# Optimization experiments

Hardware: AMD Instinct MI355X
Metric: run time of the kernel (lower is better)

Reference implementation:

```python
import jax, jax.numpy as jnp
import numpy as np

N_QUBITS = 8
N_LAYERS = 4
BATCH = 8192


def _ry_mat(theta):
    # RY(theta) = [[cos(t/2), -sin(t/2)], [sin(t/2), cos(t/2)]]; theta scalar or (B,)
    c = jnp.cos(theta * 0.5)
    s = jnp.sin(theta * 0.5)
    return jnp.stack([jnp.stack([c, -s], -1), jnp.stack([s, c], -1)], -2).astype(jnp.complex64)


def _apply_1q(state, U, wire):
    # U: (2,2) gate shared across batch; state: (B, 2,...,2) with axis wire+1 = target wire
    s = jnp.moveaxis(state, wire + 1, -1)
    s = jnp.einsum('ij,...j->...i', U, s)
    return jnp.moveaxis(s, -1, wire + 1)


def _apply_1q_batched(state, U, wire):
    # U: (B,2,2) per-sample gate (data-dependent RY angles)
    s = jnp.moveaxis(state, wire + 1, -1)
    s = jnp.einsum('bij,b...j->b...i', U, s)
    return jnp.moveaxis(s, -1, wire + 1)


def _apply_rz(state, theta, wire):
    # RZ is diagonal: multiply amplitudes by exp(-i t/2) / exp(+i t/2)
    phases = jnp.stack([jnp.exp(-0.5j * theta), jnp.exp(0.5j * theta)]).astype(jnp.complex64)
    s = jnp.moveaxis(state, wire + 1, -1)
    s = s * phases
    return jnp.moveaxis(s, -1, wire + 1)


def _cnot(state, c, t):
    # flip target amplitudes on the control=1 subspace
    s = jnp.moveaxis(state, (c + 1, t + 1), (-2, -1))
    s = jnp.stack([s[..., 0, :], s[..., 1, ::-1]], axis=-2)
    return jnp.moveaxis(s, (-2, -1), (c + 1, t + 1))


def _forward(x, weights):
    B = x.shape[0]
    state = jnp.zeros((B,) + (2,) * N_QUBITS, jnp.complex64)
    state = state.at[(slice(None),) + (0,) * N_QUBITS].set(1.0)  # |0...0>
    # data-encoding RY layer (angles depend on inputs -> per-sample gates)
    for i in range(N_QUBITS):
        state = _apply_1q_batched(state, _ry_mat(x[:, i] + weights[0, i, 0]), i)
    # entangling + rotation layers
    for layer in range(N_LAYERS):
        for i in range(N_QUBITS - 1):
            state = _cnot(state, i, i + 1)
        state = _cnot(state, N_QUBITS - 1, 0)
        for i in range(N_QUBITS):
            state = _apply_rz(state, weights[layer, i, 1], i)
            state = _apply_1q(state, _ry_mat(weights[layer, i, 0]), i)
    # <Z_i> = p(wire_i = 0) - p(wire_i = 1)
    p = state.real ** 2 + state.imag ** 2
    all_axes = tuple(range(1, N_QUBITS + 1))
    outs = []
    for i in range(N_QUBITS):
        m = p.sum(axis=tuple(a for a in all_axes if a != i + 1))  # (B, 2)
        outs.append(m[:, 0] - m[:, 1])
    return jnp.stack(outs, axis=1)  # (B, N_QUBITS)


def setup_inputs() -> dict:
    key = jax.random.key(0)
    k1, k2 = jax.random.split(key)
    x = jax.random.normal(k1, (BATCH, N_QUBITS), jnp.float32)
    weights = jax.random.normal(k2, (N_LAYERS, N_QUBITS, 2), jnp.float32)
    return {"x": x, "weights": weights}


def reference(x, weights):
    return _forward(x, weights)
```

## Files before the change

kernel.cpp:

```cpp
#include <hip/hip_runtime.h>

#define BATCH 8192

typedef __attribute__((ext_vector_type(8))) short bf16x8;
typedef __attribute__((ext_vector_type(4))) float f32x4;

__device__ __forceinline__ unsigned short f2bf(float f) {
    unsigned int u = __float_as_uint(f);
    u += 0x7fffu + ((u >> 16) & 1u);
    return (unsigned short)(u >> 16);
}
__device__ __forceinline__ float rfl(float v) {
    return __int_as_float(__builtin_amdgcn_readfirstlane(__float_as_int(v)));
}

__global__ __launch_bounds__(256) void ukern(const float* __restrict__ w,
                                             unsigned short* __restrict__ Ub)
{
    const int l = threadIdx.x & 63;
    const int c = blockIdx.x * 4 + (threadIdx.x >> 6);
    float re[4], im[4];
    const bool ls = (l == (c >> 2));
    #pragma unroll
    for (int k = 0; k < 4; ++k) {
        re[k] = (ls && ((c & 3) == k)) ? 1.0f : 0.0f;
        im[k] = 0.0f;
    }
    const int  src = (l ^ (l >> 1)) & 63;
    const bool c5  = (l & 1);
    #pragma unroll 1
    for (int layer = 0; layer < 4; ++layer) {
        const float* wl = w + layer * 16;
        float tr[4], ti[4];
        #pragma unroll
        for (int k = 0; k < 4; ++k) {
            tr[k] = __shfl(re[k], src, 64);
            ti[k] = __shfl(im[k], src, 64);
        }
        re[0] = c5 ? tr[2] : tr[0];  im[0] = c5 ? ti[2] : ti[0];
        re[1] = c5 ? tr[3] : tr[1];  im[1] = c5 ? ti[3] : ti[1];
        re[2] = c5 ? tr[1] : tr[3];  im[2] = c5 ? ti[1] : ti[3];
        re[3] = c5 ? tr[0] : tr[2];  im[3] = c5 ? ti[0] : ti[2];
        re[1] = __shfl_xor(re[1], 32, 64); im[1] = __shfl_xor(im[1], 32, 64);
        re[3] = __shfl_xor(re[3], 32, 64); im[3] = __shfl_xor(im[3], 32, 64);
        #pragma unroll
        for (int i = 0; i < 6; ++i) {
            float cth = __cosf(0.5f * wl[2*i]),   sth = __sinf(0.5f * wl[2*i]);
            float cph = __cosf(0.5f * wl[2*i+1]), sph = __sinf(0.5f * wl[2*i+1]);
            float Ar = rfl(cth * cph), SZ = rfl(sth * sph);
            float sgn = (l & (32 >> i)) ? 1.0f : -1.0f;
            float Ai = sgn * rfl(cth * sph);
            float Br = sgn * rfl(sth * cph);
            const int m = 32 >> i;
            #pragma unroll
            for (int k = 0; k < 4; ++k) {
                float br = __shfl_xor(re[k], m, 64);
                float bi = __shfl_xor(im[k], m, 64);
                float ar = re[k], ai = im[k];
                re[k] = Ar*ar - Ai*ai + Br*br + SZ*bi;
                im[k] = Ar*ai + Ai*ar + Br*bi - SZ*br;
            }
        }
        #pragma unroll
        for (int i = 0; i < 2; ++i) {
            float cy = rfl(__cosf(0.5f * wl[12 + 2*i]));
            float sy = rfl(__sinf(0.5f * wl[12 + 2*i]));
            float cf = rfl(__cosf(wl[13 + 2*i]));
            float sf = rfl(__sinf(wl[13 + 2*i]));
            const int mk = 2 >> i;
            #pragma unroll
            for (int k = 0; k < 4; ++k) {
                if (!(k & mk)) continue;
                float r = re[k], q = im[k];
                re[k] = r * cf - q * sf;
                im[k] = q * cf + r * sf;
            }
            #pragma unroll
            for (int k = 0; k < 4; ++k) {
                if (k & mk) continue;
                int k1 = k | mk;
                float ar = re[k], ai = im[k], br = re[k1], bi = im[k1];
                re[k]  = cy * ar - sy * br;
                im[k]  = cy * ai - sy * bi;
                re[k1] = sy * ar + cy * br;
                im[k1] = sy * ai + cy * bi;
            }
        }
    }
    #pragma unroll
    for (int k = 0; k < 4; ++k) {
        int i = l * 4 + k;
        Ub[i * 256 + c]         = f2bf(re[k]);
        Ub[(256 + i) * 256 + c] = f2bf(im[k]);
    }
}

__global__ __launch_bounds__(512) void qmain(const float* __restrict__ x,
                                             const float* __restrict__ w,
                                             const unsigned short* __restrict__ Ub,
                                             float* __restrict__ out)
{
    __shared__ float trg[32][17];
    __shared__ unsigned short psi[32 * 264];
    __shared__ float Ps[32][289];
    const int tid  = threadIdx.x;
    const int wid  = tid >> 6;
    const int lane = tid & 63;
    const int bid  = blockIdx.x;
    const int s0   = bid * 32;

    if (tid < 256) {
        const int s  = tid >> 3;
        const int wi = tid & 7;
        float a = 0.5f * (x[(s0 + s) * 8 + wi] + w[2 * wi]);
        trg[s][wi]     = __cosf(a);
        trg[s][8 + wi] = __sinf(a);
    }
    __syncthreads();

    {
        const int s  = tid >> 4;
        const int j1 = tid & 15;
        float c0 = trg[s][0], c1 = trg[s][1], c2 = trg[s][2], c3 = trg[s][3];
        float s0w = trg[s][8], s1w = trg[s][9], s2w = trg[s][10], s3w = trg[s][11];
        float A1 = ((j1 & 8) ? s0w : c0) * ((j1 & 4) ? s1w : c1)
                 * ((j1 & 2) ? s2w : c2) * ((j1 & 1) ? s3w : c3);
        float c4 = trg[s][4], c5 = trg[s][5], c6 = trg[s][6], c7 = trg[s][7];
        float s4 = trg[s][12], s5 = trg[s][13], s6 = trg[s][14], s7 = trg[s][15];
        float q45[4] = {A1 * c4 * c5, A1 * c4 * s5, A1 * s4 * c5, A1 * s4 * s5};
        float p67[4] = {c6 * c7, c6 * s7, s6 * c7, s6 * s7};
        unsigned int wbuf[8];
        #pragma unroll
        for (int p = 0; p < 8; ++p) {
            int ja = 2 * p, jb = 2 * p + 1;
            float va = q45[ja >> 2] * p67[ja & 3];
            float vb = q45[jb >> 2] * p67[jb & 3];
            wbuf[p] = (unsigned int)f2bf(va) | ((unsigned int)f2bf(vb) << 16);
        }
        uint4* dst = (uint4*)((char*)psi + s * 528 + j1 * 32);
        dst[0] = make_uint4(wbuf[0], wbuf[1], wbuf[2], wbuf[3]);
        dst[1] = make_uint4(wbuf[4], wbuf[5], wbuf[6], wbuf[7]);
    }
    __syncthreads();

    const int mrow = lane & 15;
    const int kgrp = lane >> 4;

    f32x4 acc[4][2];
    #pragma unroll
    for (int a = 0; a < 4; ++a)
        #pragma unroll
        for (int b = 0; b < 2; ++b)
            acc[a][b] = (f32x4){0.f, 0.f, 0.f, 0.f};

    #pragma unroll
    for (int ks = 0; ks < 8; ++ks) {
        const int k0 = ks * 32 + kgrp * 8;
        bf16x8 bfr0 = *(const bf16x8*)(psi + mrow * 264 + k0);
        bf16x8 bfr1 = *(const bf16x8*)(psi + (16 + mrow) * 264 + k0);
        #pragma unroll
        for (int mt = 0; mt < 4; ++mt) {
            const int row = (mt < 2) ? (wid * 32 + mt * 16 + mrow)
                                     : (256 + wid * 32 + (mt - 2) * 16 + mrow);
            bf16x8 afr = *(const bf16x8*)(Ub + row * 256 + k0);
            acc[mt][0] = __builtin_amdgcn_mfma_f32_16x16x32_bf16(afr, bfr0, acc[mt][0], 0, 0, 0);
            acc[mt][1] = __builtin_amdgcn_mfma_f32_16x16x32_bf16(afr, bfr1, acc[mt][1], 0, 0, 0);
        }
    }

    const int ct = wid * 4 + kgrp;
    #pragma unroll
    for (int nt = 0; nt < 2; ++nt) {
        float am[2], r2m[2], r1m[2];
        #pragma unroll
        for (int mtl = 0; mtl < 2; ++mtl) {
            float p0 = acc[mtl][nt][0]*acc[mtl][nt][0] + acc[mtl+2][nt][0]*acc[mtl+2][nt][0];
            float p1 = acc[mtl][nt][1]*acc[mtl][nt][1] + acc[mtl+2][nt][1]*acc[mtl+2][nt][1];
            float p2 = acc[mtl][nt][2]*acc[mtl][nt][2] + acc[mtl+2][nt][2]*acc[mtl+2][nt][2];
            float p3 = acc[mtl][nt][3]*acc[mtl][nt][3] + acc[mtl+2][nt][3]*acc[mtl+2][nt][3];
            float t0 = p0 + p1, t1 = p2 + p3;
            am[mtl]  = t0 + t1;
            r2m[mtl] = t0 - t1;
            r1m[mtl] = (p0 - p1) + (p2 - p3);
        }
        float ps = am[0] + am[1];
        float m3 = am[0] - am[1];
        float m6 = r2m[0] + r2m[1];
        float m7 = r1m[0] + r1m[1];
        float m0 = (wid & 4)  ? -ps : ps;
        float m1 = (wid & 2)  ? -ps : ps;
        float m2 = (wid & 1)  ? -ps : ps;
        float m4 = (kgrp & 2) ? -ps : ps;
        float m5 = (kgrp & 1) ? -ps : ps;
        const int snt = nt * 16 + mrow;
        float* pp = &Ps[ct][snt * 9];
        pp[0]=m0; pp[1]=m1; pp[2]=m2; pp[3]=m3; pp[4]=m4; pp[5]=m5; pp[6]=m6; pp[7]=m7;
    }
    __syncthreads();
    if (tid < 64) {
        const int s    = tid & 31;
        const int half = tid >> 5;
        float r0 = 0.f, r1 = 0.f, r2 = 0.f, r3 = 0.f;
        #pragma unroll
        for (int uu = 0; uu < 32; ++uu) {
            const float* pp = &Ps[uu][s * 9 + half * 4];
            r0 += pp[0]; r1 += pp[1]; r2 += pp[2]; r3 += pp[3];
        }
        float4* o = (float4*)(out + (s0 + s) * 8 + half * 4);
        *o = make_float4(r0, r1, r2, r3);
    }
}

extern "C" void kernel_launch(void* const* d_in, const int* in_sizes, int n_in,
                              void* d_out, int out_size, void* d_ws, size_t ws_size,
                              hipStream_t stream)
{
    const float* x = (const float*)d_in[0];
    const float* w = (const float*)d_in[1];
    unsigned short* Ub = (unsigned short*)d_ws;
    ukern<<<64, 256, 0, stream>>>(w, Ub);
    qmain<<<256, 512, 0, stream>>>(x, w, Ub, (float*)d_out);
}
```

Measured before the change: 23.43 us.

## Precompute gate trig per lane in ukern and reduce measurements with wave shuffles

In ukern, each lane now computes the cos/sin products for one (layer, wire) pair up front, and the gate loop fetches them with readlane. This replaces the scalar-load plus transcendental work that was repeated per gate, and the layer loop is fully unrolled. ukern is relaunched as 256 single-wave blocks instead of 64 blocks of four waves. In qmain, the cross-kgroup partial sums are reduced with xor shuffles before the shared-memory write, so the Ps buffer and the final serial reduction loop shrink fourfold at the cost of extra shuffles.

```diff
diff --git a/kernel.cpp b/kernel.cpp
--- a/kernel.cpp
+++ b/kernel.cpp
@@ -10,15 +10,38 @@
     u += 0x7fffu + ((u >> 16) & 1u);
     return (unsigned short)(u >> 16);
 }
-__device__ __forceinline__ float rfl(float v) {
-    return __int_as_float(__builtin_amdgcn_readfirstlane(__float_as_int(v)));
-}
-
-__global__ __launch_bounds__(256) void ukern(const float* __restrict__ w,
-                                             unsigned short* __restrict__ Ub)
+__device__ __forceinline__ float rdl(float v, int lane) {
+    return __int_as_float(__builtin_amdgcn_readlane(__float_as_int(v), lane));
+}
+
+__global__ __launch_bounds__(64) void ukern(const float* __restrict__ w,
+                                            unsigned short* __restrict__ Ub)
 {
-    const int l = threadIdx.x & 63;
-    const int c = blockIdx.x * 4 + (threadIdx.x >> 6);
+    const int l = threadIdx.x;
+    const int c = blockIdx.x;
+
+    float v0, v1, v2, v3;
+    {
+        const int t  = l & 31;
+        const int li = t >> 3;
+        const int wi = t & 7;
+        float th = w[(li * 8 + wi) * 2 + 0];
+        float ph = w[(li * 8 + wi) * 2 + 1];
+        float cth = __cosf(0.5f * th), sth = __sinf(0.5f * th);
+        if (wi < 6) {
+            float cph = __cosf(0.5f * ph), sph = __sinf(0.5f * ph);
+            v0 = cth * cph;
+            v1 = cth * sph;
+            v2 = sth * cph;
+            v3 = sth * sph;
+        } else {
+            v0 = cth;
+            v1 = sth;
+            v2 = __cosf(ph);
+            v3 = __sinf(ph);
+        }
+    }
+
     float re[4], im[4];
     const bool ls = (l == (c >> 2));
     #pragma unroll
@@ -28,9 +51,10 @@
     }
     const int  src = (l ^ (l >> 1)) & 63;
     const bool c5  = (l & 1);
-    #pragma unroll 1
+
+    #pragma unroll
     for (int layer = 0; layer < 4; ++layer) {
-        const float* wl = w + layer * 16;
+        const int lb = layer * 8;
         float tr[4], ti[4];
         #pragma unroll
         for (int k = 0; k < 4; ++k) {
@@ -43,14 +67,14 @@
         re[3] = c5 ? tr[0] : tr[2];  im[3] = c5 ? ti[0] : ti[2];
         re[1] = __shfl_xor(re[1], 32, 64); im[1] = __shfl_xor(im[1], 32, 64);
         re[3] = __shfl_xor(re[3], 32, 64); im[3] = __shfl_xor(im[3], 32, 64);
+
         #pragma unroll
         for (int i = 0; i < 6; ++i) {
-            float cth = __cosf(0.5f * wl[2*i]),   sth = __sinf(0.5f * wl[2*i]);
-            float cph = __cosf(0.5f * wl[2*i+1]), sph = __sinf(0.5f * wl[2*i+1]);
-            float Ar = rfl(cth * cph), SZ = rfl(sth * sph);
+            float Ar = rdl(v0, lb + i);
+            float SZ = rdl(v3, lb + i);
             float sgn = (l & (32 >> i)) ? 1.0f : -1.0f;
-            float Ai = sgn * rfl(cth * sph);
-            float Br = sgn * rfl(sth * cph);
+            float Ai = sgn * rdl(v1, lb + i);
+            float Br = sgn * rdl(v2, lb + i);
             const int m = 32 >> i;
             #pragma unroll
             for (int k = 0; k < 4; ++k) {
@@ -63,10 +87,10 @@
         }
         #pragma unroll
         for (int i = 0; i < 2; ++i) {
-            float cy = rfl(__cosf(0.5f * wl[12 + 2*i]));
-            float sy = rfl(__sinf(0.5f * wl[12 + 2*i]));
-            float cf = rfl(__cosf(wl[13 + 2*i]));
-            float sf = rfl(__sinf(wl[13 + 2*i]));
+            float cy = rdl(v0, lb + 6 + i);
+            float sy = rdl(v1, lb + 6 + i);
+            float cf = rdl(v2, lb + 6 + i);
+            float sf = rdl(v3, lb + 6 + i);
             const int mk = 2 >> i;
             #pragma unroll
             for (int k = 0; k < 4; ++k) {
@@ -102,7 +126,7 @@
 {
     __shared__ float trg[32][17];
     __shared__ unsigned short psi[32 * 264];
-    __shared__ float Ps[32][289];
+    __shared__ float Ps[8][289];
     const int tid  = threadIdx.x;
     const int wid  = tid >> 6;
     const int lane = tid & 63;
@@ -168,7 +192,6 @@
         }
     }
 
-    const int ct = wid * 4 + kgrp;
     #pragma unroll
     for (int nt = 0; nt < 2; ++nt) {
         float am[2], r2m[2], r1m[2];
@@ -192,9 +215,19 @@
         float m2 = (wid & 1)  ? -ps : ps;
         float m4 = (kgrp & 2) ? -ps : ps;
         float m5 = (kgrp & 1) ? -ps : ps;
-        const int snt = nt * 16 + mrow;
-        float* pp = &Ps[ct][snt * 9];
-        pp[0]=m0; pp[1]=m1; pp[2]=m2; pp[3]=m3; pp[4]=m4; pp[5]=m5; pp[6]=m6; pp[7]=m7;
+        m0 += __shfl_xor(m0, 16, 64);  m0 += __shfl_xor(m0, 32, 64);
+        m1 += __shfl_xor(m1, 16, 64);  m1 += __shfl_xor(m1, 32, 64);
+        m2 += __shfl_xor(m2, 16, 64);  m2 += __shfl_xor(m2, 32, 64);
+        m3 += __shfl_xor(m3, 16, 64);  m3 += __shfl_xor(m3, 32, 64);
+        m4 += __shfl_xor(m4, 16, 64);  m4 += __shfl_xor(m4, 32, 64);
+        m5 += __shfl_xor(m5, 16, 64);  m5 += __shfl_xor(m5, 32, 64);
+        m6 += __shfl_xor(m6, 16, 64);  m6 += __shfl_xor(m6, 32, 64);
+        m7 += __shfl_xor(m7, 16, 64);  m7 += __shfl_xor(m7, 32, 64);
+        if (kgrp == 0) {
+            const int snt = nt * 16 + mrow;
+            float* pp = &Ps[wid][snt * 9];
+            pp[0]=m0; pp[1]=m1; pp[2]=m2; pp[3]=m3; pp[4]=m4; pp[5]=m5; pp[6]=m6; pp[7]=m7;
+        }
     }
     __syncthreads();
     if (tid < 64) {
@@ -202,7 +235,7 @@
         const int half = tid >> 5;
         float r0 = 0.f, r1 = 0.f, r2 = 0.f, r3 = 0.f;
         #pragma unroll
-        for (int uu = 0; uu < 32; ++uu) {
+        for (int uu = 0; uu < 8; ++uu) {
             const float* pp = &Ps[uu][s * 9 + half * 4];
             r0 += pp[0]; r1 += pp[1]; r2 += pp[2]; r3 += pp[3];
         }
@@ -218,6 +251,6 @@
     const float* x = (const float*)d_in[0];
     const float* w = (const float*)d_in[1];
     unsigned short* Ub = (unsigned short*)d_ws;
-    ukern<<<64, 256, 0, stream>>>(w, Ub);
+    ukern<<<256, 64, 0, stream>>>(w, Ub);
     qmain<<<256, 512, 0, stream>>>(x, w, Ub, (float*)d_out);
 }
```

Measured after the change: 22.15 us. 5.5% less time.
